# Performance work log

Measured on AMD Instinct MI355X. Metric: run time of the kernel, lower is better.

The kernel has to match this reference:

```python
import jax, jax.numpy as jnp
import numpy as np

U_NUM, I_NUM, F_DIM, N_EDGES, BATCH = 50000, 20000, 64, 1000000, 131072
T = 1.0  # temperature

def setup_inputs() -> dict:
    key = jax.random.key(0)
    ks = jax.random.split(key, 16)
    return {
        'embed_user': jax.random.normal(ks[0], (U_NUM, F_DIM), jnp.float32) * 0.01,
        'embed_item': jax.random.normal(ks[1], (I_NUM, F_DIM), jnp.float32) * 0.01,
        'old_U_emb': jax.random.normal(ks[2], (U_NUM, F_DIM), jnp.float32),
        'old_I_emb': jax.random.normal(ks[3], (I_NUM, F_DIM), jnp.float32),
        'edge_rows': jax.random.randint(ks[4], (N_EDGES,), 0, U_NUM, jnp.int32),
        'edge_cols': jax.random.randint(ks[5], (N_EDGES,), 0, I_NUM, jnp.int32),
        'ui_vals': jax.random.uniform(ks[6], (N_EDGES,), jnp.float32),
        'iu_vals': jax.random.uniform(ks[7], (N_EDGES,), jnp.float32),
        'user': jax.random.randint(ks[8], (BATCH,), 0, U_NUM, jnp.int32),
        'item_i': jax.random.randint(ks[9], (BATCH,), 0, U_NUM, jnp.int32),
        'item_j': jax.random.randint(ks[10], (BATCH,), 0, U_NUM, jnp.int32),
        'degree_U': jax.random.uniform(ks[11], (BATCH,), jnp.float32),
        'item_z_U': jax.random.randint(ks[12], (BATCH,), 0, U_NUM, jnp.int32),
        'user_': jax.random.randint(ks[13], (BATCH,), 0, I_NUM, jnp.int32),
        'item_i_': jax.random.randint(ks[14], (BATCH,), 0, I_NUM, jnp.int32),
        'item_j_': jax.random.randint(ks[15], (BATCH,), 0, I_NUM, jnp.int32),
        'degree_I': jax.random.uniform(jax.random.fold_in(key, 99), (BATCH,), jnp.float32),
        'item_z_I': jax.random.randint(jax.random.fold_in(key, 98), (BATCH,), 0, I_NUM, jnp.int32),
    }

def _spmm_ui(vals, rows, cols, item_emb):
    # (U x I sparse) @ item_emb -> [U, F]
    return jax.ops.segment_sum(vals[:, None] * item_emb[cols], rows, num_segments=U_NUM)

def _spmm_iu(vals, rows, cols, user_emb):
    # (I x U sparse) @ user_emb -> [I, F]
    return jax.ops.segment_sum(vals[:, None] * user_emb[rows], cols, num_segments=I_NUM)

def _contrastive(idx_u, idx_i, idx_j, degree, num, old_emb, gcn_emb):
    u = old_emb[idx_u]            # [B, F]
    pi = gcn_emb[idx_i]           # [B, F]
    pj = gcn_emb[idx_j]           # [B, F]
    si = jnp.sum(u * pi, axis=-1) / T
    sj = jnp.sum(u * pj, axis=-1) / T
    # -log(exp(si) / (exp(sj) + exp(si))) = logaddexp(si, sj) - si  (stable form)
    log_ratio = si - jnp.logaddexp(si, sj)
    return -jnp.sum(log_ratio * degree) / num

def reference(embed_user, embed_item, old_U_emb, old_I_emb, ui_vals, iu_vals,
              degree_U, degree_I, edge_rows, edge_cols,
              user, item_i, item_j, item_z_U, user_, item_i_, item_j_, item_z_I):
    u0, i0 = embed_user, embed_item
    u1 = _spmm_ui(ui_vals, edge_rows, edge_cols, i0)
    i1 = _spmm_iu(iu_vals, edge_rows, edge_cols, u0)
    u2 = _spmm_ui(ui_vals, edge_rows, edge_cols, i1)
    i2 = _spmm_iu(iu_vals, edge_rows, edge_cols, u1)
    u3 = _spmm_ui(ui_vals, edge_rows, edge_cols, i2)
    i3 = _spmm_iu(iu_vals, edge_rows, edge_cols, u2)
    gcn_u = u0 + 0.5 * u1 + (1.0 / 3.0) * u2 + 0.25 * u3
    gcn_i = i0 + 0.5 * i1 + (1.0 / 3.0) * i2 + 0.25 * i3
    loss = _contrastive(user, item_i, item_j, degree_U, U_NUM, old_U_emb, gcn_u)
    loss = loss + _contrastive(user_, item_i_, item_j_, degree_I, I_NUM, old_I_emb, gcn_i)
    return loss
```

## Files before the change

### kernel.cpp

```cpp
#include <hip/hip_runtime.h>

#define U_NUM 50000
#define I_NUM 20000
#define F_DIM 64
#define N_EDGES 1000000
#define BATCH 131072

#define FP_U 200
#define FP_I 160
#define CAPF_U 5632
#define CAPF_I 6912
#define TILE 8192
#define NBU 123
#define NBI 123
#define CVB 512

#if defined(__has_builtin)
#if __has_builtin(__builtin_amdgcn_cvt_pk_f32_fp8) && __has_builtin(__builtin_amdgcn_cvt_pk_fp8_f32)
#define HW_FP8 1
#endif
#endif

typedef float v2f __attribute__((ext_vector_type(2)));

__device__ __forceinline__ void dec4(unsigned u, float* f) {
#ifdef HW_FP8
    v2f lo = __builtin_amdgcn_cvt_pk_f32_fp8((int)u, false);
    v2f hi = __builtin_amdgcn_cvt_pk_f32_fp8((int)u, true);
    f[0] = lo.x; f[1] = lo.y; f[2] = hi.x; f[3] = hi.y;
#else
    #pragma unroll
    for (int i = 0; i < 4; i++) {
        unsigned v = (u >> (8 * i)) & 0xFFu;
        unsigned s = v >> 7, e = (v >> 3) & 15u, m = v & 7u;
        float mag = (e == 0) ? (float)m * 0.001953125f
                             : __uint_as_float(((e + 120u) << 23) | (m << 20));
        f[i] = s ? -mag : mag;
    }
#endif
}

#ifndef HW_FP8
__device__ __forceinline__ unsigned char enc1(float x) {
    unsigned s = (__float_as_uint(x) >> 31) << 7;
    float a = fabsf(x);
    if (a >= 448.f) return (unsigned char)(s | 0x7E);
    if (a < 0.015625f) {
        int m = __float2int_rn(a * 512.f);
        if (m >= 8) return (unsigned char)(s | 0x08);
        return (unsigned char)(s | m);
    }
    unsigned au = __float_as_uint(a);
    au += 0x7FFFFu + ((au >> 20) & 1u);
    int e = (int)(au >> 23) - 127;
    if (e > 8) return (unsigned char)(s | 0x7E);
    return (unsigned char)(s | ((unsigned)(e + 7) << 3) | ((au >> 20) & 7u));
}
#endif

__device__ __forceinline__ unsigned enc4(float a, float b, float c, float d) {
#ifdef HW_FP8
    int v = __builtin_amdgcn_cvt_pk_fp8_f32(a, b, 0, false);
    v = __builtin_amdgcn_cvt_pk_fp8_f32(c, d, v, true);
    return (unsigned)v;
#else
    return (unsigned)enc1(a) | ((unsigned)enc1(b) << 8)
         | ((unsigned)enc1(c) << 16) | ((unsigned)enc1(d) << 24);
#endif
}

__device__ __forceinline__ unsigned short f2b(float f) {
    unsigned b = __float_as_uint(f);
    b += 0x7FFFu + ((b >> 16) & 1u);
    return (unsigned short)(b >> 16);
}

#define N_EU 800000
#define N_EI 320000
#define N_OU 800000
#define N_OI 320000
#define CVT_TOT (N_EU + N_EI + N_OU + N_OI)
__global__ void build_fine(const int* __restrict__ rows, const int* __restrict__ cols,
                           const float* __restrict__ uiv, const float* __restrict__ iuv,
                           int* __restrict__ fcurU, int2* __restrict__ fbufU,
                           int* __restrict__ fcurI, int2* __restrict__ fbufI,
                           const float* __restrict__ eU, const float* __restrict__ eI,
                           const float* __restrict__ oU, const float* __restrict__ oI,
                           unsigned* __restrict__ e8U, unsigned* __restrict__ e8I,
                           unsigned* __restrict__ o8U, unsigned* __restrict__ o8I)
{
    if (blockIdx.x >= NBU + NBI) {
        for (int idx = (blockIdx.x - NBU - NBI) * 256 + threadIdx.x;
             idx < CVT_TOT; idx += CVB * 256) {
            const float* s; unsigned* d; int off; float sc;
            if (idx < N_EU)                      { s = eU; d = e8U; off = idx; sc = 128.f; }
            else if (idx < N_EU + N_EI)          { s = eI; d = e8I; off = idx - N_EU; sc = 128.f; }
            else if (idx < N_EU + N_EI + N_OU)   { s = oU; d = o8U; off = idx - N_EU - N_EI; sc = 1.f; }
            else                                 { s = oI; d = o8I; off = idx - N_EU - N_EI - N_OU; sc = 1.f; }
            float4 v = ((const float4*)s)[off];
            d[off] = enc4(v.x * sc, v.y * sc, v.z * sc, v.w * sc);
        }
        return;
    }

    __shared__ int2 rec[TILE];
    __shared__ unsigned char pid[TILE];
    __shared__ int hist[256], scan[256], curs[256], delta[256];

    bool isU = blockIdx.x < NBU;
    int tb = isU ? blockIdx.x : blockIdx.x - NBU;
    int n0 = tb * TILE;
    int n  = min(TILE, N_EDGES - n0);
    int bins  = isU ? FP_U : FP_I;
    int capf  = isU ? CAPF_U : CAPF_I;
    int shift = isU ? 8 : 7;
    int* fcur = isU ? fcurU : fcurI;
    int2* fbuf = isU ? fbufU : fbufI;
    const int* keys = isU ? rows : cols;
    const int* srcs = isU ? cols : rows;
    const float* vals = isU ? uiv : iuv;

    hist[threadIdx.x] = 0;
    __syncthreads();

    for (int t = threadIdx.x; t < n; t += 256)
        atomicAdd(&hist[keys[n0 + t] >> shift], 1);
    __syncthreads();

    int v = hist[threadIdx.x];
    scan[threadIdx.x] = v;
    __syncthreads();
    for (int off = 1; off < 256; off <<= 1) {
        int t = ((int)threadIdx.x >= off) ? scan[threadIdx.x - off] : 0;
        __syncthreads();
        scan[threadIdx.x] += t;
        __syncthreads();
    }
    int lbase = scan[threadIdx.x] - v;
    curs[threadIdx.x] = lbase;
    if ((int)threadIdx.x < bins) {
        int res = v ? atomicAdd(&fcur[threadIdx.x], v) : 0;
        delta[threadIdx.x] = threadIdx.x * capf + res - lbase;
    }
    __syncthreads();

    for (int t = threadIdx.x; t < n; t += 256) {
        int key = keys[n0 + t];
        int src = srcs[n0 + t];
        float vv = vals[n0 + t];
        int b = key >> shift;
        int slot = atomicAdd(&curs[b], 1);
        int2 r;
        r.x = (int)(((unsigned)src << 16) | (unsigned)key);
        r.y = __float_as_int(vv);
        rec[slot] = r;
        pid[slot] = (unsigned char)b;
    }
    __syncthreads();

    for (int t = threadIdx.x; t < n; t += 256) {
        int b = pid[t];
        int a = delta[b] + t;
        if (a < (b + 1) * capf) fbuf[a] = rec[t];
    }
}

__global__ void sort_csr(const int* __restrict__ fcurU, const int2* __restrict__ fbufU,
                         int* __restrict__ ptrU, int* __restrict__ cntU, unsigned* __restrict__ edgesU,
                         const int* __restrict__ fcurI, const int2* __restrict__ fbufI,
                         int* __restrict__ ptrI, int* __restrict__ cntI, unsigned* __restrict__ edgesI)
{
    __shared__ int hist[256], scan[256], curs[256];
    __shared__ int gbase_s;

    const int* fcur; const int2* fbuf; int* ptr; int* cnt; unsigned* edges;
    int fp, bins, capf, nrow;
    if (blockIdx.x < FP_U) {
        fcur = fcurU; fbuf = fbufU; ptr = ptrU; cnt = cntU; edges = edgesU;
        fp = blockIdx.x; bins = 256; capf = CAPF_U; nrow = U_NUM;
    } else {
        fcur = fcurI; fbuf = fbufI; ptr = ptrI; cnt = cntI; edges = edgesI;
        fp = blockIdx.x - FP_U; bins = 128; capf = CAPF_I; nrow = I_NUM;
    }

    if (threadIdx.x == 0) gbase_s = 0;
    for (int i = threadIdx.x; i < bins; i += 256) hist[i] = 0;
    __syncthreads();

    int contrib = ((int)threadIdx.x < fp) ? min(fcur[threadIdx.x], capf) : 0;
    #pragma unroll
    for (int off = 32; off > 0; off >>= 1) contrib += __shfl_down(contrib, off, 64);
    if ((threadIdx.x & 63) == 0 && contrib) atomicAdd(&gbase_s, contrib);

    int n = min(fcur[fp], capf);
    const int2* src = fbuf + (size_t)fp * capf;
    int mask = bins - 1;

    for (int t = threadIdx.x; t < n; t += 256) {
        int dst = src[t].x & 0xFFFF;
        atomicAdd(&hist[dst & mask], 1);
    }
    __syncthreads();

    int v = ((int)threadIdx.x < bins) ? hist[threadIdx.x] : 0;
    scan[threadIdx.x] = v;
    __syncthreads();
    for (int off = 1; off < 256; off <<= 1) {
        int t = ((int)threadIdx.x >= off) ? scan[threadIdx.x - off] : 0;
        __syncthreads();
        scan[threadIdx.x] += t;
        __syncthreads();
    }
    int ex = scan[threadIdx.x] - v;
    curs[threadIdx.x] = ex;
    __syncthreads();
    int gbase = gbase_s;

    if ((int)threadIdx.x < bins) {
        int row = fp * bins + threadIdx.x;
        if (row < nrow) {
            ptr[row] = gbase + ex;
            cnt[row] = v;
        }
    }

    for (int t = threadIdx.x; t < n; t += 256) {
        int2 r = src[t];
        int dst = r.x & 0xFFFF;
        int pos = atomicAdd(&curs[dst & mask], 1);
        unsigned rec = ((unsigned)f2b(__int_as_float(r.y)) << 16)
                     | ((unsigned)r.x >> 16);
        edges[gbase + pos] = rec;
    }
}

template <int MODE>
__global__ void spmm_level(const int* __restrict__ ptrU, const int* __restrict__ cntU,
                           const unsigned* __restrict__ edgesU, const unsigned* __restrict__ srcU,
                           unsigned* __restrict__ dstU,
                           const unsigned* __restrict__ l0U, const unsigned* __restrict__ l1U,
                           const unsigned* __restrict__ l2U, unsigned* __restrict__ g8U,
                           const int* __restrict__ ptrI, const int* __restrict__ cntI,
                           const unsigned* __restrict__ edgesI, const unsigned* __restrict__ srcI,
                           unsigned* __restrict__ dstI,
                           const unsigned* __restrict__ l0I, const unsigned* __restrict__ l1I,
                           const unsigned* __restrict__ l2I, unsigned* __restrict__ g8I)
{
    int wave = (blockIdx.x * blockDim.x + threadIdx.x) >> 6;
    bool isU = wave >= I_NUM;
    int row = isU ? wave - I_NUM : wave;
    if (isU && row >= U_NUM) return;

    const int*  ptr   = isU ? ptrU   : ptrI;
    const int*  cnt   = isU ? cntU   : cntI;
    const unsigned* edges = isU ? edgesU : edgesI;
    const unsigned* semb  = isU ? srcU   : srcI;

    int lane = threadIdx.x & 63;
    int sub  = lane >> 4;
    int q    = lane & 15;
    int begin = __builtin_amdgcn_readfirstlane(ptr[row]);
    int len   = __builtin_amdgcn_readfirstlane(cnt[row]);
    const unsigned* erow = edges + begin;

    float4 a0 = make_float4(0.f, 0.f, 0.f, 0.f);
    float4 a1 = make_float4(0.f, 0.f, 0.f, 0.f);
    float4 a2 = make_float4(0.f, 0.f, 0.f, 0.f);
    float4 a3 = make_float4(0.f, 0.f, 0.f, 0.f);
    int k = sub;
    for (; k + 12 < len; k += 16) {
        unsigned r0 = erow[k];
        unsigned r1 = erow[k + 4];
        unsigned r2 = erow[k + 8];
        unsigned r3 = erow[k + 12];
        unsigned x0 = semb[((size_t)(r0 & 0xFFFFu) << 4) + q];
        unsigned x1 = semb[((size_t)(r1 & 0xFFFFu) << 4) + q];
        unsigned x2 = semb[((size_t)(r2 & 0xFFFFu) << 4) + q];
        unsigned x3 = semb[((size_t)(r3 & 0xFFFFu) << 4) + q];
        float v0 = __uint_as_float(r0 & 0xFFFF0000u);
        float v1 = __uint_as_float(r1 & 0xFFFF0000u);
        float v2 = __uint_as_float(r2 & 0xFFFF0000u);
        float v3 = __uint_as_float(r3 & 0xFFFF0000u);
        float f0[4], f1[4], f2[4], f3[4];
        dec4(x0, f0); dec4(x1, f1); dec4(x2, f2); dec4(x3, f3);
        a0.x += v0 * f0[0]; a0.y += v0 * f0[1]; a0.z += v0 * f0[2]; a0.w += v0 * f0[3];
        a1.x += v1 * f1[0]; a1.y += v1 * f1[1]; a1.z += v1 * f1[2]; a1.w += v1 * f1[3];
        a2.x += v2 * f2[0]; a2.y += v2 * f2[1]; a2.z += v2 * f2[2]; a2.w += v2 * f2[3];
        a3.x += v3 * f3[0]; a3.y += v3 * f3[1]; a3.z += v3 * f3[2]; a3.w += v3 * f3[3];
    }
    for (; k < len; k += 4) {
        unsigned r0 = erow[k];
        unsigned x0 = semb[((size_t)(r0 & 0xFFFFu) << 4) + q];
        float v0 = __uint_as_float(r0 & 0xFFFF0000u);
        float f0[4];
        dec4(x0, f0);
        a0.x += v0 * f0[0]; a0.y += v0 * f0[1]; a0.z += v0 * f0[2]; a0.w += v0 * f0[3];
    }
    float4 acc;
    acc.x = (a0.x + a1.x) + (a2.x + a3.x);
    acc.y = (a0.y + a1.y) + (a2.y + a3.y);
    acc.z = (a0.z + a1.z) + (a2.z + a3.z);
    acc.w = (a0.w + a1.w) + (a2.w + a3.w);

    acc.x += __shfl_xor(acc.x, 16, 64);
    acc.y += __shfl_xor(acc.y, 16, 64);
    acc.z += __shfl_xor(acc.z, 16, 64);
    acc.w += __shfl_xor(acc.w, 16, 64);
    acc.x += __shfl_xor(acc.x, 32, 64);
    acc.y += __shfl_xor(acc.y, 32, 64);
    acc.z += __shfl_xor(acc.z, 32, 64);
    acc.w += __shfl_xor(acc.w, 32, 64);

    if (sub == 0) {
        size_t ro = ((size_t)row << 4) + q;
        if (MODE < 2) {
            unsigned* dst = isU ? dstU : dstI;
            dst[ro] = enc4(acc.x, acc.y, acc.z, acc.w);
        } else {
            const unsigned* l0 = isU ? l0U : l0I;
            const unsigned* l1 = isU ? l1U : l1I;
            const unsigned* l2 = isU ? l2U : l2I;
            unsigned* g8       = isU ? g8U : g8I;
            float e[4], b[4], c[4];
            dec4(l0[ro], e); dec4(l1[ro], b); dec4(l2[ro], c);
            const float third = 1.f / 3.f;
            float gx = 0.125f * (e[0] + 0.5f * b[0] + third * c[0] + 0.25f * acc.x);
            float gy = 0.125f * (e[1] + 0.5f * b[1] + third * c[1] + 0.25f * acc.y);
            float gz = 0.125f * (e[2] + 0.5f * b[2] + third * c[2] + 0.25f * acc.z);
            float gw = 0.125f * (e[3] + 0.5f * b[3] + third * c[3] + 0.25f * acc.w);
            g8[ro] = enc4(gx, gy, gz, gw);
        }
    }
}

__device__ __forceinline__ float dotq(const float* a, const float* b) {
    return a[0] * b[0] + a[1] * b[1] + a[2] * b[2] + a[3] * b[3];
}

__global__ void __launch_bounds__(256, 2)
contrastive_side(const unsigned* __restrict__ oldU, const unsigned* __restrict__ gcnU,
                 const int* __restrict__ userU, const int* __restrict__ iiU,
                 const int* __restrict__ ijU, const float* __restrict__ degU,
                 const unsigned* __restrict__ oldI, const unsigned* __restrict__ gcnI,
                 const int* __restrict__ userI, const int* __restrict__ iiI,
                 const int* __restrict__ ijI, const float* __restrict__ degI,
                 float* __restrict__ out)
{
    const int HALF = 2048;
    bool isU = blockIdx.x < HALF;
    const unsigned* old_ = isU ? oldU : oldI;
    const unsigned* gcn_ = isU ? gcnU : gcnI;
    const int* pu_  = isU ? userU : userI;
    const int* pii  = isU ? iiU   : iiI;
    const int* pij  = isU ? ijU   : ijI;
    const float* pdg = isU ? degU : degI;
    float inv = isU ? (1.f / U_NUM) : (1.f / I_NUM);
    int bid = isU ? blockIdx.x : blockIdx.x - HALF;

    int lane = threadIdx.x & 63;
    int sub  = lane >> 4;
    int ql   = lane & 15;
    int qg = (bid * blockDim.x + threadIdx.x) >> 4;
    int s0 = qg << 2;

    int sel = ql >> 2, so = s0 + (ql & 3);
    const int* p = (sel == 0) ? (pu_ + so) : (sel == 1) ? (pii + so)
                 : (sel == 2) ? (pij + so) : ((const int*)pdg + so);
    int idx = *p;

    int qb = sub << 4;
    unsigned Au[4], Ai[4], Aj[4];
    #pragma unroll
    for (int t = 0; t < 4; t++) {
        int u = __shfl(idx, qb + t, 64);
        int i = __shfl(idx, qb + 4 + t, 64);
        int j = __shfl(idx, qb + 8 + t, 64);
        Au[t] = old_[((size_t)u << 4) + ql];
        Ai[t] = gcn_[((size_t)i << 4) + ql];
        Aj[t] = gcn_[((size_t)j << 4) + ql];
    }

    float si[4], sj[4];
    #pragma unroll
    for (int t = 0; t < 4; t++) {
        float fu[4], fi[4], fj[4];
        dec4(Au[t], fu); dec4(Ai[t], fi); dec4(Aj[t], fj);
        si[t] = dotq(fu, fi); sj[t] = dotq(fu, fj);
    }

    #pragma unroll
    for (int off = 1; off < 16; off <<= 1) {
        #pragma unroll
        for (int t = 0; t < 4; t++) {
            si[t] += __shfl_xor(si[t], off, 64);
            sj[t] += __shfl_xor(sj[t], off, 64);
        }
    }

    int t3 = ql & 3;
    float siv = si[t3];
    float sjv = sj[t3];
    float dg = __int_as_float(__shfl(idx, qb + 12 + t3, 64));

    const float S = 0.0625f;
    siv *= S; sjv *= S;
    float m = fmaxf(siv, sjv);
    float lse = m + logf(expf(siv - m) + expf(sjv - m));
    float acc = (ql < 4) ? -(siv - lse) * dg * inv : 0.f;

    #pragma unroll
    for (int off = 32; off > 0; off >>= 1) acc += __shfl_down(acc, off, 64);
    __shared__ float wsum[4];
    if (lane == 0) wsum[threadIdx.x >> 6] = acc;
    __syncthreads();
    if (threadIdx.x == 0)
        atomicAdd(out, wsum[0] + wsum[1] + wsum[2] + wsum[3]);
}

extern "C" void kernel_launch(void* const* d_in, const int* in_sizes, int n_in,
                              void* d_out, int out_size, void* d_ws, size_t ws_size,
                              hipStream_t stream)
{
    const float* embed_user = (const float*)d_in[0];
    const float* embed_item = (const float*)d_in[1];
    const float* old_U      = (const float*)d_in[2];
    const float* old_I      = (const float*)d_in[3];
    const int*   erow       = (const int*)d_in[4];
    const int*   ecol       = (const int*)d_in[5];
    const float* ui_vals    = (const float*)d_in[6];
    const float* iu_vals    = (const float*)d_in[7];
    const int*   user       = (const int*)d_in[8];
    const int*   item_i     = (const int*)d_in[9];
    const int*   item_j     = (const int*)d_in[10];
    const float* degU       = (const float*)d_in[11];
    const int*   user_      = (const int*)d_in[13];
    const int*   item_i_    = (const int*)d_in[14];
    const int*   item_j_    = (const int*)d_in[15];
    const float* degI       = (const float*)d_in[16];

    const size_t UF = (size_t)U_NUM * F_DIM;
    const size_t IF = (size_t)I_NUM * F_DIM;
    const size_t FRECU = (size_t)FP_U * CAPF_U;
    const size_t FRECI = (size_t)FP_I * CAPF_I;

    int2*  fbufU  = (int2*)d_ws;
    int2*  fbufI  = fbufU + FRECU;
    unsigned* edgesU = (unsigned*)(fbufI + FRECI);
    unsigned* edgesI = edgesU + N_EDGES;
    char* cur = (char*)(edgesI + N_EDGES);
    unsigned* e8U = (unsigned*)cur; cur += UF;
    unsigned* e8I = (unsigned*)cur; cur += IF;
    unsigned* o8U = (unsigned*)cur; cur += UF;
    unsigned* o8I = (unsigned*)cur; cur += IF;
    unsigned* u1_8 = (unsigned*)cur; cur += UF;
    unsigned* u2_8 = (unsigned*)cur; cur += UF;
    unsigned* i1_8 = (unsigned*)cur; cur += IF;
    unsigned* i2_8 = (unsigned*)cur; cur += IF;
    unsigned* g8U  = (unsigned*)cur; cur += UF;
    unsigned* g8I  = (unsigned*)cur; cur += IF;
    int* fcurU = (int*)cur;
    int* fcurI = fcurU + 256;
    int* ptrU  = fcurI + 256;
    int* cntUa = ptrU + U_NUM;
    int* ptrI  = cntUa + U_NUM;
    int* cntIa = ptrI + I_NUM;

    dim3 blk(256);
    const int bf_blocks  = NBU + NBI + CVB;
    const int st_blocks  = FP_U + FP_I;
    const int spmm_blocks = (U_NUM + I_NUM) / 4;

    hipMemsetAsync(fcurU, 0, 512 * sizeof(int), stream);
    hipMemsetAsync(d_out, 0, sizeof(float), stream);

    build_fine<<<bf_blocks, blk, 0, stream>>>(erow, ecol, ui_vals, iu_vals,
                                              fcurU, fbufU, fcurI, fbufI,
                                              embed_user, embed_item, old_U, old_I,
                                              e8U, e8I, o8U, o8I);
    sort_csr<<<st_blocks, blk, 0, stream>>>(fcurU, fbufU, ptrU, cntUa, edgesU,
                                            fcurI, fbufI, ptrI, cntIa, edgesI);

    spmm_level<0><<<spmm_blocks, blk, 0, stream>>>(
        ptrU, cntUa, edgesU, e8I, u1_8, nullptr, nullptr, nullptr, nullptr,
        ptrI, cntIa, edgesI, e8U, i1_8, nullptr, nullptr, nullptr, nullptr);
    spmm_level<1><<<spmm_blocks, blk, 0, stream>>>(
        ptrU, cntUa, edgesU, i1_8, u2_8, nullptr, nullptr, nullptr, nullptr,
        ptrI, cntIa, edgesI, u1_8, i2_8, nullptr, nullptr, nullptr, nullptr);
    spmm_level<2><<<spmm_blocks, blk, 0, stream>>>(
        ptrU, cntUa, edgesU, i2_8, nullptr, e8U, u1_8, u2_8, g8U,
        ptrI, cntIa, edgesI, u2_8, nullptr, e8I, i1_8, i2_8, g8I);

    contrastive_side<<<4096, blk, 0, stream>>>(o8U, g8U, user, item_i, item_j, degU,
                                               o8I, g8I, user_, item_i_, item_j_, degI,
                                               (float*)d_out);
}
```

Baseline: 321.7 us.

## Use gfx950 scaled FP8 converts, reorder SpMM waves, double contrastive samples per thread

Adds a code path that uses the gfx950 scalef32 FP8 pack/unpack builtins when they are available, falling back to the older gfx940 builtins otherwise. The SpMM level kernel now assigns the first waves to user rows and the later waves to item rows, which changes dispatch order. The contrastive kernel processes 8 samples per 16-lane group instead of 4, halving the grid and raising memory-level parallelism per thread at the cost of more registers.

```diff
diff --git a/kernel.cpp b/kernel.cpp
--- a/kernel.cpp
+++ b/kernel.cpp
@@ -15,16 +15,23 @@
 #define NBI 123
 #define CVB 512
 
+typedef float v2f __attribute__((ext_vector_type(2)));
+typedef short v2s __attribute__((ext_vector_type(2)));
+
 #if defined(__has_builtin)
-#if __has_builtin(__builtin_amdgcn_cvt_pk_f32_fp8) && __has_builtin(__builtin_amdgcn_cvt_pk_fp8_f32)
-#define HW_FP8 1
+#if __has_builtin(__builtin_amdgcn_cvt_scalef32_pk_f32_fp8) && __has_builtin(__builtin_amdgcn_cvt_scalef32_pk_fp8_f32)
+#define HW_FP8_950 1
+#elif __has_builtin(__builtin_amdgcn_cvt_pk_f32_fp8) && __has_builtin(__builtin_amdgcn_cvt_pk_fp8_f32)
+#define HW_FP8_940 1
 #endif
 #endif
 
-typedef float v2f __attribute__((ext_vector_type(2)));
-
 __device__ __forceinline__ void dec4(unsigned u, float* f) {
-#ifdef HW_FP8
+#if defined(HW_FP8_950)
+    v2f lo = __builtin_amdgcn_cvt_scalef32_pk_f32_fp8(u, 1.0f, false);
+    v2f hi = __builtin_amdgcn_cvt_scalef32_pk_f32_fp8(u, 1.0f, true);
+    f[0] = lo.x; f[1] = lo.y; f[2] = hi.x; f[3] = hi.y;
+#elif defined(HW_FP8_940)
     v2f lo = __builtin_amdgcn_cvt_pk_f32_fp8((int)u, false);
     v2f hi = __builtin_amdgcn_cvt_pk_f32_fp8((int)u, true);
     f[0] = lo.x; f[1] = lo.y; f[2] = hi.x; f[3] = hi.y;
@@ -40,7 +47,7 @@
 #endif
 }
 
-#ifndef HW_FP8
+#if !defined(HW_FP8_950) && !defined(HW_FP8_940)
 __device__ __forceinline__ unsigned char enc1(float x) {
     unsigned s = (__float_as_uint(x) >> 31) << 7;
     float a = fabsf(x);
@@ -59,7 +66,13 @@
 #endif
 
 __device__ __forceinline__ unsigned enc4(float a, float b, float c, float d) {
-#ifdef HW_FP8
+#if defined(HW_FP8_950)
+    union { v2s s; unsigned u; } r;
+    r.s.x = 0; r.s.y = 0;
+    r.s = __builtin_amdgcn_cvt_scalef32_pk_fp8_f32(r.s, a, b, 1.0f, false);
+    r.s = __builtin_amdgcn_cvt_scalef32_pk_fp8_f32(r.s, c, d, 1.0f, true);
+    return r.u;
+#elif defined(HW_FP8_940)
     int v = __builtin_amdgcn_cvt_pk_fp8_f32(a, b, 0, false);
     v = __builtin_amdgcn_cvt_pk_fp8_f32(c, d, v, true);
     return (unsigned)v;
@@ -247,9 +260,9 @@
                            const unsigned* __restrict__ l2I, unsigned* __restrict__ g8I)
 {
     int wave = (blockIdx.x * blockDim.x + threadIdx.x) >> 6;
-    bool isU = wave >= I_NUM;
-    int row = isU ? wave - I_NUM : wave;
-    if (isU && row >= U_NUM) return;
+    bool isU = wave < U_NUM;
+    int row = isU ? wave : wave - U_NUM;
+    if (!isU && row >= I_NUM) return;
 
     const int*  ptr   = isU ? ptrU   : ptrI;
     const int*  cnt   = isU ? cntU   : cntI;
@@ -337,16 +350,22 @@
     return a[0] * b[0] + a[1] * b[1] + a[2] * b[2] + a[3] * b[3];
 }
 
+__device__ __forceinline__ float sel4f(float a, float b, float c, float d, int k) {
+    float lo = (k & 1) ? b : a;
+    float hi = (k & 1) ? d : c;
+    return (k & 2) ? hi : lo;
+}
+
 __global__ void __launch_bounds__(256, 2)
-contrastive_side(const unsigned* __restrict__ oldU, const unsigned* __restrict__ gcnU,
-                 const int* __restrict__ userU, const int* __restrict__ iiU,
-                 const int* __restrict__ ijU, const float* __restrict__ degU,
-                 const unsigned* __restrict__ oldI, const unsigned* __restrict__ gcnI,
-                 const int* __restrict__ userI, const int* __restrict__ iiI,
-                 const int* __restrict__ ijI, const float* __restrict__ degI,
-                 float* __restrict__ out)
+contrastive_side8(const unsigned* __restrict__ oldU, const unsigned* __restrict__ gcnU,
+                  const int* __restrict__ userU, const int* __restrict__ iiU,
+                  const int* __restrict__ ijU, const float* __restrict__ degU,
+                  const unsigned* __restrict__ oldI, const unsigned* __restrict__ gcnI,
+                  const int* __restrict__ userI, const int* __restrict__ iiI,
+                  const int* __restrict__ ijI, const float* __restrict__ degI,
+                  float* __restrict__ out)
 {
-    const int HALF = 2048;
+    const int HALF = 1024;
     bool isU = blockIdx.x < HALF;
     const unsigned* old_ = isU ? oldU : oldI;
     const unsigned* gcn_ = isU ? gcnU : gcnI;
@@ -361,28 +380,31 @@
     int sub  = lane >> 4;
     int ql   = lane & 15;
     int qg = (bid * blockDim.x + threadIdx.x) >> 4;
-    int s0 = qg << 2;
-
-    int sel = ql >> 2, so = s0 + (ql & 3);
-    const int* p = (sel == 0) ? (pu_ + so) : (sel == 1) ? (pii + so)
-                 : (sel == 2) ? (pij + so) : ((const int*)pdg + so);
-    int idx = *p;
+    int s0 = qg << 3;
+
+    int sel = ql >> 2;
+    const int* p = (sel == 0) ? ((const int*)pu_) : (sel == 1) ? ((const int*)pii)
+                 : (sel == 2) ? ((const int*)pij) : ((const int*)pdg);
+    p += s0 + (ql & 3);
+    int idxA = p[0];
+    int idxB = p[4];
 
     int qb = sub << 4;
-    unsigned Au[4], Ai[4], Aj[4];
+    unsigned Au[8], Ai[8], Aj[8];
     #pragma unroll
-    for (int t = 0; t < 4; t++) {
-        int u = __shfl(idx, qb + t, 64);
-        int i = __shfl(idx, qb + 4 + t, 64);
-        int j = __shfl(idx, qb + 8 + t, 64);
+    for (int t = 0; t < 8; t++) {
+        int src = (t < 4) ? idxA : idxB;
+        int u = __shfl(src, qb + (t & 3), 64);
+        int i = __shfl(src, qb + 4 + (t & 3), 64);
+        int j = __shfl(src, qb + 8 + (t & 3), 64);
         Au[t] = old_[((size_t)u << 4) + ql];
         Ai[t] = gcn_[((size_t)i << 4) + ql];
         Aj[t] = gcn_[((size_t)j << 4) + ql];
     }
 
-    float si[4], sj[4];
+    float si[8], sj[8];
     #pragma unroll
-    for (int t = 0; t < 4; t++) {
+    for (int t = 0; t < 8; t++) {
         float fu[4], fi[4], fj[4];
         dec4(Au[t], fu); dec4(Ai[t], fi); dec4(Aj[t], fj);
         si[t] = dotq(fu, fi); sj[t] = dotq(fu, fj);
@@ -391,22 +413,27 @@
     #pragma unroll
     for (int off = 1; off < 16; off <<= 1) {
         #pragma unroll
-        for (int t = 0; t < 4; t++) {
+        for (int t = 0; t < 8; t++) {
             si[t] += __shfl_xor(si[t], off, 64);
             sj[t] += __shfl_xor(sj[t], off, 64);
         }
     }
 
     int t3 = ql & 3;
-    float siv = si[t3];
-    float sjv = sj[t3];
-    float dg = __int_as_float(__shfl(idx, qb + 12 + t3, 64));
+    float dgA = __int_as_float(__shfl(idxA, qb + 12 + t3, 64));
+    float dgB = __int_as_float(__shfl(idxB, qb + 12 + t3, 64));
+    bool hi4 = (ql & 4) != 0;
+    float siv = hi4 ? sel4f(si[4], si[5], si[6], si[7], t3)
+                    : sel4f(si[0], si[1], si[2], si[3], t3);
+    float sjv = hi4 ? sel4f(sj[4], sj[5], sj[6], sj[7], t3)
+                    : sel4f(sj[0], sj[1], sj[2], sj[3], t3);
+    float dg = hi4 ? dgB : dgA;
 
     const float S = 0.0625f;
     siv *= S; sjv *= S;
     float m = fmaxf(siv, sjv);
     float lse = m + logf(expf(siv - m) + expf(sjv - m));
-    float acc = (ql < 4) ? -(siv - lse) * dg * inv : 0.f;
+    float acc = (ql < 8) ? -(siv - lse) * dg * inv : 0.f;
 
     #pragma unroll
     for (int off = 32; off > 0; off >>= 1) acc += __shfl_down(acc, off, 64);
@@ -490,7 +517,7 @@
         ptrU, cntUa, edgesU, i2_8, nullptr, e8U, u1_8, u2_8, g8U,
         ptrI, cntIa, edgesI, u2_8, nullptr, e8I, i1_8, i2_8, g8I);
 
-    contrastive_side<<<4096, blk, 0, stream>>>(o8U, g8U, user, item_i, item_j, degU,
-                                               o8I, g8I, user_, item_i_, item_j_, degI,
-                                               (float*)d_out);
-}
+    contrastive_side8<<<2048, blk, 0, stream>>>(o8U, g8U, user, item_i, item_j, degU,
+                                                o8I, g8I, user_, item_i_, item_j_, degI,
+                                                (float*)d_out);
+}
```

Result: faster. 297.6 us (-7.5%).
